# Kernel tuning notes

Measured on AMD Instinct MI355X. Metric: run time of the kernel, lower is better.

## Reference

```python
import jax, jax.numpy as jnp
import numpy as np

D_K = 64

def setup_inputs() -> dict:
    key = jax.random.key(0)
    ks = jax.random.split(key, 9)
    B, S, D = 8, 2048, 512
    d_k, d_v = 64, 64
    return {
        "q_in": jax.random.normal(ks[0], (B, S, D), jnp.float32),
        "k_in": jax.random.normal(ks[1], (B, S, D), jnp.float32),
        "v_in": jax.random.normal(ks[2], (B, S, D), jnp.float32),
        "Wq": jax.random.normal(ks[3], (D, d_k), jnp.float32) * 0.05,
        "bq": jax.random.normal(ks[4], (d_k,), jnp.float32) * 0.05,
        "Wk": jax.random.normal(ks[5], (D, d_k), jnp.float32) * 0.05,
        "bk": jax.random.normal(ks[6], (d_k,), jnp.float32) * 0.05,
        "Wv": jax.random.normal(ks[7], (D, d_v), jnp.float32) * 0.05,
        "bv": jax.random.normal(ks[8], (d_v,), jnp.float32) * 0.05,
    }

def reference(q_in, k_in, v_in, Wq, bq, Wk, bk, Wv, bv):
    # Dense projections: x @ W + b
    q = jnp.einsum('bsd,dk->bsk', q_in, Wq) + bq  # [B,S,d_k]
    k = jnp.einsum('bsd,dk->bsk', k_in, Wk) + bk  # [B,S,d_k]
    v = jnp.einsum('bsd,dv->bsv', v_in, Wv) + bv  # [B,S,d_v]
    scale = 1.0 / np.sqrt(D_K).astype(np.float32)
    scores = jnp.einsum('bqk,bsk->bqs', q, k) * scale  # [B,S,S]
    attn = jax.nn.softmax(scores, axis=-1)
    return jnp.einsum('bqs,bsv->bqv', attn, v)  # [B,S,d_v]
```

## Files before the change

### kernel.cpp

```cpp
#include <hip/hip_runtime.h>
#include <hip/hip_bf16.h>
#include <cstdint>

typedef __attribute__((ext_vector_type(8))) short short8;
typedef __attribute__((ext_vector_type(16))) float f32x16;

#if __has_builtin(__builtin_amdgcn_exp2f)
#define EXP2F(x) __builtin_amdgcn_exp2f(x)
#else
#define EXP2F(x) exp2f(x)
#endif

#define MFMA32(A, B, C) __builtin_amdgcn_mfma_f32_32x32x16_bf16((A), (B), (C), 0, 0, 0)

__device__ __forceinline__ unsigned short f2bf(float f) {
  unsigned int u = __builtin_bit_cast(unsigned int, f);
  u += 0x7FFFu + ((u >> 16) & 1u);
  return (unsigned short)(u >> 16);
}

__device__ __forceinline__ short8 packA(const float4 &a0, const float4 &a1) {
  uint4 uu;
  uu.x = (unsigned int)f2bf(a0.x) | ((unsigned int)f2bf(a0.y) << 16);
  uu.y = (unsigned int)f2bf(a0.z) | ((unsigned int)f2bf(a0.w) << 16);
  uu.z = (unsigned int)f2bf(a1.x) | ((unsigned int)f2bf(a1.y) << 16);
  uu.w = (unsigned int)f2bf(a1.z) | ((unsigned int)f2bf(a1.w) << 16);
  return __builtin_bit_cast(short8, uu);
}

__global__ __launch_bounds__(256) void prep_wt(
    const float* __restrict__ Wq, const float* __restrict__ Wk,
    const float* __restrict__ Wv, unsigned short* __restrict__ Wt)
{
  int idx = blockIdx.x * 256 + threadIdx.x;
  int which = idx >> 15;
  int rem = idx & 32767;
  int n = rem >> 9;
  int k = rem & 511;
  const float* W = (which == 0) ? Wq : (which == 1) ? Wk : Wv;
  Wt[idx] = f2bf(W[k * 64 + n]);
}

__global__ __launch_bounds__(256) void proj_kernel(
    const float* __restrict__ qin, const float* __restrict__ kin,
    const float* __restrict__ vin, const unsigned short* __restrict__ Wt,
    const float* __restrict__ bq, const float* __restrict__ bk,
    const float* __restrict__ bv,
    unsigned short* __restrict__ Qo, unsigned short* __restrict__ Ko,
    unsigned short* __restrict__ Vto)
{
  __shared__ float Xf[2][64 * 64];

  const int which = blockIdx.y;
  const float* X    = (which == 0) ? qin : (which == 1) ? kin : vin;
  const float* bias = (which == 0) ? bq  : (which == 1) ? bk  : bv;

  const int tid = threadIdx.x;
  const int lane = tid & 63, wv = tid >> 6;
  const int h = lane >> 5, l31 = lane & 31;
  const int grp = wv & 1, nh = wv >> 1;
  const int m0 = blockIdx.x * 64;

  const unsigned short* wcol =
      Wt + (size_t)which * 32768 + (size_t)(nh * 32 + l31) * 512 + h * 8;

  const int srow4 = tid >> 4;
  const int sslot = tid & 15;

  auto stage = [&](int chunk, int buf) {
    #pragma unroll
    for (int k = 0; k < 4; ++k) {
      const int row = k * 16 + srow4;
      const int l = sslot ^ (row & 15);
      const float* gp = X + (size_t)(m0 + row) * 512 + chunk * 64 + l * 4;
      char* lp = (char*)&Xf[buf][0] + k * 4096 + wv * 1024;
      __builtin_amdgcn_global_load_lds(
          (const __attribute__((address_space(1))) unsigned int*)gp,
          (__attribute__((address_space(3))) unsigned int*)lp, 16, 0, 0);
    }
  };

  stage(0, 0);
  __syncthreads();

  f32x16 acc = {};
  int buf = 0;
  #pragma unroll
  for (int c = 0; c < 8; ++c) {
    if (c < 7) stage(c + 1, buf ^ 1);
    const int r = grp * 32 + l31;
    const float* arow = &Xf[buf][r * 64];
    const int rx = r & 15;
    const unsigned short* wk = wcol + c * 64;
    #pragma unroll
    for (int ks = 0; ks < 4; ++ks) {
      const int s0 = ks * 4 + h * 2;
      float4 x0 = *(const float4*)(arow + ((s0 ^ rx) * 4));
      float4 x1 = *(const float4*)(arow + (((s0 + 1) ^ rx) * 4));
      short8 af = packA(x0, x1);
      short8 bf = *(const short8*)(wk + ks * 16);
      acc = MFMA32(af, bf, acc);
    }
    __syncthreads();
    buf ^= 1;
  }

  const float bv0 = bias[nh * 32 + l31];

  if (which < 2) {
    const float scale = which ? 1.0f : 0.18033688f;
    unsigned short* Y = which ? Ko : Qo;
    #pragma unroll
    for (int r = 0; r < 16; ++r) {
      int row = (r & 3) + 8 * (r >> 2) + 4 * h;
      Y[(size_t)(m0 + grp * 32 + row) * 64 + nh * 32 + l31] =
          f2bf((acc[r] + bv0) * scale);
    }
  } else {
    __syncthreads();
    unsigned short* TB = (unsigned short*)&Xf[0][0];
    #pragma unroll
    for (int r = 0; r < 16; ++r) {
      int row = (r & 3) + 8 * (r >> 2) + 4 * h;
      TB[(nh * 32 + l31) * 68 + grp * 32 + row] = f2bf(acc[r] + bv0);
    }
    __syncthreads();
    int bidx = blockIdx.x >> 5;
    int s0 = (blockIdx.x & 31) * 64;
    for (int i = tid; i < 64 * 16; i += 256) {
      int n = i >> 4, cs = i & 15;
      ushort4 v4 = *(const ushort4*)(TB + n * 68 + cs * 4);
      *(ushort4*)(Vto + ((size_t)bidx * 64 + n) * 2048 + s0 + cs * 4) = v4;
    }
  }
}

__global__ __launch_bounds__(512, 2) void attn_kernel(
    const unsigned short* __restrict__ Q, const unsigned short* __restrict__ K,
    const unsigned short* __restrict__ Vt, float* __restrict__ out)
{
  __shared__ float ObS[4][16][64];
  __shared__ float MpS[4][64];
  __shared__ float LpS[4][64];

  const int tid = threadIdx.x;
  const int lane = tid & 63, w = tid >> 6;
  const int h = lane >> 5, l31 = lane & 31;
  const int b = blockIdx.y;
  const int q0 = blockIdx.x * 64;

  short8 qf[2][4];
  #pragma unroll
  for (int qt = 0; qt < 2; ++qt) {
    const unsigned short* qp = Q + ((size_t)(b * 2048 + q0 + qt * 32 + l31)) * 64 + h * 8;
    #pragma unroll
    for (int c = 0; c < 4; ++c) qf[qt][c] = *(const short8*)(qp + c * 16);
  }

  f32x16 o00 = {}, o01 = {}, o10 = {}, o11 = {};
  float m0 = -1e30f, m1 = -1e30f, ls0 = 0.f, ls1 = 0.f;

  const unsigned short* Kp  = K  + ((size_t)(b * 2048 + w * 256 + l31)) * 64 + h * 8;
  const unsigned short* Vp0 = Vt + ((size_t)(b * 64 + l31)) * 2048 + w * 256 + h * 8;
  const unsigned short* Vp1 = Vp0 + (size_t)32 * 2048;

  short8 kf[4], vf0[2], vf1[2];
  #pragma unroll
  for (int c = 0; c < 4; ++c) kf[c] = *(const short8*)(Kp + c * 16);
  vf0[0] = *(const short8*)(Vp0); vf0[1] = *(const short8*)(Vp0 + 16);
  vf1[0] = *(const short8*)(Vp1); vf1[1] = *(const short8*)(Vp1 + 16);

  auto process = [&](f32x16 sT, float &m, float &ls, f32x16 &oA, f32x16 &oB) {
    float tm[8];
    #pragma unroll
    for (int i = 0; i < 8; ++i) tm[i] = fmaxf(sT[2 * i], sT[2 * i + 1]);
    #pragma unroll
    for (int i = 0; i < 4; ++i) tm[i] = fmaxf(tm[i], tm[i + 4]);
    float mx = fmaxf(fmaxf(tm[0], tm[1]), fmaxf(tm[2], tm[3]));
    mx = fmaxf(mx, __shfl_xor(mx, 32, 64));
    if (__any(mx > m + 8.0f)) {
      float mnew = fmaxf(m, mx);
      float alpha = EXP2F(m - mnew);
      m = mnew;
      ls *= alpha; oA *= alpha; oB *= alpha;
    }
    float p[16];
    #pragma unroll
    for (int r = 0; r < 16; ++r) p[r] = EXP2F(sT[r] - m);
    float ts[8];
    #pragma unroll
    for (int i = 0; i < 8; ++i) ts[i] = p[2 * i] + p[2 * i + 1];
    #pragma unroll
    for (int i = 0; i < 4; ++i) ts[i] += ts[i + 4];
    float rs = (ts[0] + ts[1]) + (ts[2] + ts[3]);
    rs += __shfl_xor(rs, 32, 64);
    ls += rs;
    unsigned int pk[8];
    #pragma unroll
    for (int i = 0; i < 8; ++i)
      pk[i] = (unsigned int)f2bf(p[2 * i]) | ((unsigned int)f2bf(p[2 * i + 1]) << 16);
    unsigned int ex[8];
    #pragma unroll
    for (int i = 0; i < 8; ++i) ex[i] = (unsigned int)__shfl_xor((int)pk[i], 32, 64);
    uint4 cc0, cc1;
    if (h == 0) { cc0 = make_uint4(pk[0], pk[1], ex[0], ex[1]); cc1 = make_uint4(pk[4], pk[5], ex[4], ex[5]); }
    else        { cc0 = make_uint4(ex[2], ex[3], pk[2], pk[3]); cc1 = make_uint4(ex[6], ex[7], pk[6], pk[7]); }
    short8 P0 = __builtin_bit_cast(short8, cc0);
    short8 P1 = __builtin_bit_cast(short8, cc1);
    __builtin_amdgcn_s_setprio(1);
    oA = MFMA32(vf0[0], P0, oA); oA = MFMA32(vf0[1], P1, oA);
    oB = MFMA32(vf1[0], P0, oB); oB = MFMA32(vf1[1], P1, oB);
    __builtin_amdgcn_s_setprio(0);
  };

  for (int st = 0; st < 8; ++st) {
    f32x16 s0 = {}, s1 = {};
    __builtin_amdgcn_s_setprio(1);
    #pragma unroll
    for (int c = 0; c < 4; ++c) s0 = MFMA32(kf[c], qf[0][c], s0);
    #pragma unroll
    for (int c = 0; c < 4; ++c) s1 = MFMA32(kf[c], qf[1][c], s1);
    __builtin_amdgcn_s_setprio(0);
    if (st < 7) {
      #pragma unroll
      for (int c = 0; c < 4; ++c)
        kf[c] = *(const short8*)(Kp + (size_t)(st + 1) * 2048 + c * 16);
    }
    process(s0, m0, ls0, o00, o10);
    process(s1, m1, ls1, o01, o11);
    if (st < 7) {
      vf0[0] = *(const short8*)(Vp0 + (st + 1) * 32);
      vf0[1] = *(const short8*)(Vp0 + (st + 1) * 32 + 16);
      vf1[0] = *(const short8*)(Vp1 + (st + 1) * 32);
      vf1[1] = *(const short8*)(Vp1 + (st + 1) * 32 + 16);
    }
  }

  for (int half = 4; half > 0; half >>= 1) {
    const bool writer = (w >= half) && (w < 2 * half);
    const bool merger = (w < half);
    __syncthreads();
    if (writer && h == 0) {
      MpS[w - half][l31] = m0;      LpS[w - half][l31] = ls0;
      MpS[w - half][32 + l31] = m1; LpS[w - half][32 + l31] = ls1;
    }
    __syncthreads();
    float fb0 = 0.f, fb1 = 0.f;
    if (merger) {
      float pm0 = MpS[w][l31],      pl0 = LpS[w][l31];
      float pm1 = MpS[w][32 + l31], pl1 = LpS[w][32 + l31];
      float nm0 = fmaxf(m0, pm0), nm1 = fmaxf(m1, pm1);
      float fa0 = EXP2F(m0 - nm0); fb0 = EXP2F(pm0 - nm0);
      float fa1 = EXP2F(m1 - nm1); fb1 = EXP2F(pm1 - nm1);
      m0 = nm0; m1 = nm1;
      ls0 = ls0 * fa0 + pl0 * fb0; ls1 = ls1 * fa1 + pl1 * fb1;
      o00 *= fa0; o10 *= fa0; o01 *= fa1; o11 *= fa1;
    }
    __syncthreads();
    if (writer) {
      #pragma unroll
      for (int r = 0; r < 16; ++r) ObS[w - half][r][lane] = o00[r]; }
    __syncthreads();
    if (merger) {
      #pragma unroll
      for (int r = 0; r < 16; ++r) o00[r] += ObS[w][r][lane] * fb0; }
    __syncthreads();
    if (writer) {
      #pragma unroll
      for (int r = 0; r < 16; ++r) ObS[w - half][r][lane] = o01[r]; }
    __syncthreads();
    if (merger) {
      #pragma unroll
      for (int r = 0; r < 16; ++r) o01[r] += ObS[w][r][lane] * fb1; }
    __syncthreads();
    if (writer) {
      #pragma unroll
      for (int r = 0; r < 16; ++r) ObS[w - half][r][lane] = o10[r]; }
    __syncthreads();
    if (merger) {
      #pragma unroll
      for (int r = 0; r < 16; ++r) o10[r] += ObS[w][r][lane] * fb0; }
    __syncthreads();
    if (writer) {
      #pragma unroll
      for (int r = 0; r < 16; ++r) ObS[w - half][r][lane] = o11[r]; }
    __syncthreads();
    if (merger) {
      #pragma unroll
      for (int r = 0; r < 16; ++r) o11[r] += ObS[w][r][lane] * fb1; }
  }

  if (w == 0) {
    float i0 = 1.0f / ls0, i1 = 1.0f / ls1;
    o00 *= i0; o10 *= i0; o01 *= i1; o11 *= i1;
    #pragma unroll
    for (int qt = 0; qt < 2; ++qt) {
      int q = qt * 32 + l31;
      float* ob = out + ((size_t)(b * 2048 + q0 + q)) * 64 + 4 * h;
      const f32x16 a = qt ? o01 : o00;
      const f32x16 c = qt ? o11 : o10;
      #pragma unroll
      for (int g = 0; g < 4; ++g) {
        *(float4*)(ob + 8 * g)      = make_float4(a[4*g], a[4*g+1], a[4*g+2], a[4*g+3]);
        *(float4*)(ob + 32 + 8 * g) = make_float4(c[4*g], c[4*g+1], c[4*g+2], c[4*g+3]);
      }
    }
  }
}

extern "C" void kernel_launch(void* const* d_in, const int* in_sizes, int n_in,
                              void* d_out, int out_size, void* d_ws, size_t ws_size,
                              hipStream_t stream) {
  const float* qin = (const float*)d_in[0];
  const float* kin = (const float*)d_in[1];
  const float* vin = (const float*)d_in[2];
  const float* Wq  = (const float*)d_in[3];
  const float* bq  = (const float*)d_in[4];
  const float* Wk  = (const float*)d_in[5];
  const float* bk  = (const float*)d_in[6];
  const float* Wv  = (const float*)d_in[7];
  const float* bv  = (const float*)d_in[8];

  unsigned short* Qo  = (unsigned short*)d_ws;
  unsigned short* Ko  = Qo + (size_t)16384 * 64;
  unsigned short* Vto = Ko + (size_t)16384 * 64;
  unsigned short* Wt  = Vto + (size_t)8 * 64 * 2048;
  float* out = (float*)d_out;

  hipLaunchKernelGGL(prep_wt, dim3(384), dim3(256), 0, stream, Wq, Wk, Wv, Wt);
  hipLaunchKernelGGL(proj_kernel, dim3(256, 3), dim3(256), 0, stream,
                     qin, kin, vin, Wt, bq, bk, bv, Qo, Ko, Vto);
  hipLaunchKernelGGL(attn_kernel, dim3(32, 8), dim3(512), 0, stream, Qo, Ko, Vto, out);
}
```

Measured before the change: 163.8 us.

## Split projection K across 8 waves with triple-buffered LDS pipeline

The projection kernel now uses 512 threads: two wave groups each handle half of every K chunk, and their partial accumulators are reduced through LDS at the end. Staging moves from double to triple buffering with vmcnt-based waits and raw barriers, and all weight fragments are preloaded into registers before the loop. The goal is more memory-level parallelism and latency hiding in the bandwidth-bound projection. The cost is extra LDS, a reduction step and higher register pressure from the 16 preloaded weight fragments.

```diff
diff --git a/kernel.cpp b/kernel.cpp
--- a/kernel.cpp
+++ b/kernel.cpp
@@ -41,7 +41,7 @@
   Wt[idx] = f2bf(W[k * 64 + n]);
 }
 
-__global__ __launch_bounds__(256) void proj_kernel(
+__global__ __launch_bounds__(512, 4) void proj_kernel(
     const float* __restrict__ qin, const float* __restrict__ kin,
     const float* __restrict__ vin, const unsigned short* __restrict__ Wt,
     const float* __restrict__ bq, const float* __restrict__ bk,
@@ -49,31 +49,30 @@
     unsigned short* __restrict__ Qo, unsigned short* __restrict__ Ko,
     unsigned short* __restrict__ Vto)
 {
-  __shared__ float Xf[2][64 * 64];
+  __shared__ float Xf[3][64 * 64];
 
   const int which = blockIdx.y;
   const float* X    = (which == 0) ? qin : (which == 1) ? kin : vin;
   const float* bias = (which == 0) ? bq  : (which == 1) ? bk  : bv;
 
   const int tid = threadIdx.x;
-  const int lane = tid & 63, wv = tid >> 6;
+  const int lane = tid & 63, w = tid >> 6;
   const int h = lane >> 5, l31 = lane & 31;
-  const int grp = wv & 1, nh = wv >> 1;
+  const int qd = w & 3;
+  const int grp = qd & 1, nh = qd >> 1;
+  const int khalf = w >> 2;
   const int m0 = blockIdx.x * 64;
 
-  const unsigned short* wcol =
-      Wt + (size_t)which * 32768 + (size_t)(nh * 32 + l31) * 512 + h * 8;
-
-  const int srow4 = tid >> 4;
+  const int srow5 = tid >> 4;
   const int sslot = tid & 15;
 
   auto stage = [&](int chunk, int buf) {
     #pragma unroll
-    for (int k = 0; k < 4; ++k) {
-      const int row = k * 16 + srow4;
+    for (int k = 0; k < 2; ++k) {
+      const int row = k * 32 + srow5;
       const int l = sslot ^ (row & 15);
       const float* gp = X + (size_t)(m0 + row) * 512 + chunk * 64 + l * 4;
-      char* lp = (char*)&Xf[buf][0] + k * 4096 + wv * 1024;
+      char* lp = (char*)&Xf[buf][0] + k * 8192 + w * 1024;
       __builtin_amdgcn_global_load_lds(
           (const __attribute__((address_space(1))) unsigned int*)gp,
           (__attribute__((address_space(3))) unsigned int*)lp, 16, 0, 0);
@@ -81,53 +80,77 @@
   };
 
   stage(0, 0);
-  __syncthreads();
-
-  f32x16 acc = {};
-  int buf = 0;
+  stage(1, 1);
+  const unsigned short* wcol =
+      Wt + (size_t)which * 32768 + (size_t)(nh * 32 + l31) * 512 + h * 8;
+  short8 wf[16];
   #pragma unroll
   for (int c = 0; c < 8; ++c) {
-    if (c < 7) stage(c + 1, buf ^ 1);
-    const int r = grp * 32 + l31;
-    const float* arow = &Xf[buf][r * 64];
-    const int rx = r & 15;
-    const unsigned short* wk = wcol + c * 64;
-    #pragma unroll
-    for (int ks = 0; ks < 4; ++ks) {
+    wf[2 * c]     = *(const short8*)(wcol + c * 64 + (khalf * 2 + 0) * 16);
+    wf[2 * c + 1] = *(const short8*)(wcol + c * 64 + (khalf * 2 + 1) * 16);
+  }
+  __syncthreads();
+
+  const int r = grp * 32 + l31, rx = r & 15;
+  f32x16 acc = {};
+  #pragma unroll
+  for (int c = 0; c < 8; ++c) {
+    if (c < 6) stage(c + 2, (c + 2) % 3);
+    const float* arow = &Xf[c % 3][r * 64];
+    #pragma unroll
+    for (int j = 0; j < 2; ++j) {
+      const int ks = khalf * 2 + j;
       const int s0 = ks * 4 + h * 2;
       float4 x0 = *(const float4*)(arow + ((s0 ^ rx) * 4));
       float4 x1 = *(const float4*)(arow + (((s0 + 1) ^ rx) * 4));
       short8 af = packA(x0, x1);
-      short8 bf = *(const short8*)(wk + ks * 16);
-      acc = MFMA32(af, bf, acc);
-    }
-    __syncthreads();
-    buf ^= 1;
+      acc = MFMA32(af, wf[2 * c + j], acc);
+    }
+    if (c < 7) {
+      if (c < 6) asm volatile("s_waitcnt vmcnt(2)" ::: "memory");
+      else       asm volatile("s_waitcnt vmcnt(0)" ::: "memory");
+      __builtin_amdgcn_s_barrier();
+    }
+  }
+
+  float* scr = (float*)&Xf[0][0];
+  if (w >= 4) {
+    #pragma unroll
+    for (int t = 0; t < 16; ++t) scr[qd * 1024 + t * 64 + lane] = acc[t];
+  }
+  __syncthreads();
+  if (w < 4) {
+    #pragma unroll
+    for (int t = 0; t < 16; ++t) acc[t] += scr[qd * 1024 + t * 64 + lane];
   }
 
   const float bv0 = bias[nh * 32 + l31];
 
   if (which < 2) {
-    const float scale = which ? 1.0f : 0.18033688f;
-    unsigned short* Y = which ? Ko : Qo;
-    #pragma unroll
-    for (int r = 0; r < 16; ++r) {
-      int row = (r & 3) + 8 * (r >> 2) + 4 * h;
-      Y[(size_t)(m0 + grp * 32 + row) * 64 + nh * 32 + l31] =
-          f2bf((acc[r] + bv0) * scale);
+    if (w < 4) {
+      const float scale = which ? 1.0f : 0.18033688f;
+      unsigned short* Y = which ? Ko : Qo;
+      #pragma unroll
+      for (int t = 0; t < 16; ++t) {
+        int row = (t & 3) + 8 * (t >> 2) + 4 * h;
+        Y[(size_t)(m0 + grp * 32 + row) * 64 + nh * 32 + l31] =
+            f2bf((acc[t] + bv0) * scale);
+      }
     }
   } else {
     __syncthreads();
     unsigned short* TB = (unsigned short*)&Xf[0][0];
-    #pragma unroll
-    for (int r = 0; r < 16; ++r) {
-      int row = (r & 3) + 8 * (r >> 2) + 4 * h;
-      TB[(nh * 32 + l31) * 68 + grp * 32 + row] = f2bf(acc[r] + bv0);
+    if (w < 4) {
+      #pragma unroll
+      for (int t = 0; t < 16; ++t) {
+        int row = (t & 3) + 8 * (t >> 2) + 4 * h;
+        TB[(nh * 32 + l31) * 68 + grp * 32 + row] = f2bf(acc[t] + bv0);
+      }
     }
     __syncthreads();
     int bidx = blockIdx.x >> 5;
     int s0 = (blockIdx.x & 31) * 64;
-    for (int i = tid; i < 64 * 16; i += 256) {
+    for (int i = tid; i < 64 * 16; i += 512) {
       int n = i >> 4, cs = i & 15;
       ushort4 v4 = *(const ushort4*)(TB + n * 68 + cs * 4);
       *(ushort4*)(Vto + ((size_t)bidx * 64 + n) * 2048 + s0 + cs * 4) = v4;
@@ -328,7 +351,7 @@
   float* out = (float*)d_out;
 
   hipLaunchKernelGGL(prep_wt, dim3(384), dim3(256), 0, stream, Wq, Wk, Wv, Wt);
-  hipLaunchKernelGGL(proj_kernel, dim3(256, 3), dim3(256), 0, stream,
+  hipLaunchKernelGGL(proj_kernel, dim3(256, 3), dim3(512), 0, stream,
                      qin, kin, vin, Wt, bq, bk, bv, Qo, Ko, Vto);
   hipLaunchKernelGGL(attn_kernel, dim3(32, 8), dim3(512), 0, stream, Qo, Ko, Vto, out);
 }
```

New measurement: 166.3 us. No clear change (+1.5%).
